# Kernel optimization log

Measured on AMD Instinct MI355X. Metric: run time of the kernel, lower is better.

The kernel has to match this reference:

```python
import jax, jax.numpy as jnp
import numpy as np

SCALE = 0.08838834764831845  # 1/sqrt(head_dim=128)

T, H, D = 8192, 16, 128
NUM_SLOTS = 16384
SEQ_LEN = 2048


def setup_inputs() -> dict:
    key = jax.random.key(0)
    kq, kk, kv = jax.random.split(key, 3)
    q = jax.random.normal(kq, (T, H, D), dtype=jnp.float32)
    k = jax.random.normal(kk, (T, H, D), dtype=jnp.float32)
    v = jax.random.normal(kv, (T, H, D), dtype=jnp.float32)
    k_cache = jnp.zeros((NUM_SLOTS, H * D), dtype=jnp.float32)
    v_cache = jnp.zeros((NUM_SLOTS, H * D), dtype=jnp.float32)
    slot_mapping = jnp.arange(T, dtype=jnp.int32)  # contiguous slots; -1 would mean skip
    return {"q": q, "k": k, "v": v, "k_cache": k_cache, "v_cache": v_cache,
            "slot_mapping": slot_mapping, "seq_len": SEQ_LEN}


def reference(q, k, v, k_cache, v_cache, slot_mapping, seq_len):
    # --- store_kvcache: scatter per-token K/V rows into paged cache slots ---
    t, h, d = q.shape
    num_slots = k_cache.shape[0]
    # slot == -1 means "do not store"; remap to an out-of-bounds index and drop.
    safe_slots = jnp.where(slot_mapping < 0, num_slots, slot_mapping)
    k_cache = k_cache.at[safe_slots].set(k.reshape(t, h * d), mode="drop")
    v_cache = v_cache.at[safe_slots].set(v.reshape(t, h * d), mode="drop")

    # --- prefill attention reading K/V from the cache (block_tables path) ---
    # cu_seqlens = [0, S, 2S, ...]: equal-length sequences packed contiguously,
    # so the per-sequence cache slices are the first t rows reshaped to [B,S,H,D].
    b = t // seq_len
    qb = q.reshape(b, seq_len, h, d)
    kb = k_cache[:t].reshape(b, seq_len, h, d)
    vb = v_cache[:t].reshape(b, seq_len, h, d)

    scores = jnp.einsum("bqhd,bkhd->bhqk", qb, kb) * SCALE  # [B,H,S,S]
    causal = jnp.tril(jnp.ones((seq_len, seq_len), dtype=bool))
    scores = jnp.where(causal[None, None], scores, -jnp.inf)
    p = jax.nn.softmax(scores, axis=-1)
    o = jnp.einsum("bhqk,bkhd->bqhd", p, vb)
    return o.reshape(t, h, d)
```

## Files before the change

kernel.cpp:

```cpp
#include <hip/hip_runtime.h>

typedef float f32x16 __attribute__((ext_vector_type(16)));
typedef __bf16 bf16x8 __attribute__((ext_vector_type(8)));
typedef unsigned int uint2v __attribute__((ext_vector_type(2)));

#define Hh 16
#define Dd 128
#define SEQ 2048
#define HD 2048
#define ATT_C 0.12751743f
#define NEGINF (-__builtin_inff())

__device__ __forceinline__ ushort f2bf(float f) {
    uint u = __builtin_bit_cast(uint, f);
    return (ushort)((u + 0x7FFFu + ((u >> 16) & 1u)) >> 16);
}

__device__ __forceinline__ uint4 pack8(float4 a, float4 b) {
    uint4 u;
    u.x = (uint)f2bf(a.x) | ((uint)f2bf(a.y) << 16);
    u.y = (uint)f2bf(a.z) | ((uint)f2bf(a.w) << 16);
    u.z = (uint)f2bf(b.x) | ((uint)f2bf(b.y) << 16);
    u.w = (uint)f2bf(b.z) | ((uint)f2bf(b.w) << 16);
    return u;
}

__device__ __forceinline__ uint pkbf(float a, float b) {
    return (uint)f2bf(a) | ((uint)f2bf(b) << 16);
}

__device__ __forceinline__ f32x16 zero16() {
    f32x16 v;
#pragma unroll
    for (int i = 0; i < 16; ++i) v[i] = 0.f;
    return v;
}

__device__ __forceinline__ void gll16(const void* g, void* l) {
    __builtin_amdgcn_global_load_lds(
        (const __attribute__((address_space(1))) unsigned int*)g,
        (__attribute__((address_space(3))) unsigned int*)l, 16, 0, 0);
}

__device__ __forceinline__ bf16x8 mkfrag(uint a01, uint a23, uint a45, uint a67, int hi) {
    uint4 u;
#if __has_builtin(__builtin_amdgcn_permlane32_swap)
    uint2v xz = __builtin_amdgcn_permlane32_swap(a01, a45, false, false);
    uint2v yw = __builtin_amdgcn_permlane32_swap(a23, a67, false, false);
    u.x = xz[0]; u.y = yw[0]; u.z = xz[1]; u.w = yw[1];
    (void)hi;
#else
    uint s01 = __shfl_xor(a01, 32), s23 = __shfl_xor(a23, 32);
    uint s45 = __shfl_xor(a45, 32), s67 = __shfl_xor(a67, 32);
    u.x = hi ? s45 : a01;
    u.y = hi ? s67 : a23;
    u.z = hi ? a45 : s01;
    u.w = hi ? a67 : s23;
#endif
    return __builtin_bit_cast(bf16x8, u);
}

__global__ void initinv(int* __restrict__ inv, int T) {
    int i = blockIdx.x * 256 + threadIdx.x;
    if (i < T) inv[i] = -1;
}
__global__ void buildinv(const int* __restrict__ slots, int* __restrict__ inv, int T) {
    int t = blockIdx.x * 256 + threadIdx.x;
    if (t < T) { int s = slots[t]; if (s >= 0 && s < T) inv[s] = t; }
}

__global__ void fusekv(const float* __restrict__ k, const float* __restrict__ v,
                       const float* __restrict__ kc, const float* __restrict__ vc,
                       const int* __restrict__ inv, ushort* __restrict__ ek,
                       ushort* __restrict__ evt) {
    __shared__ int sv[64];
    __shared__ ushort Ks[64][136];
    __shared__ ushort Lt[128][72];
    const int tid = threadIdx.x;
    const int r0 = blockIdx.x * 64, h = blockIdx.y;
    const int b = r0 >> 11, tok0 = r0 & (SEQ - 1);
    const long tb = ((long)(b * Hh + h) * 32 + (tok0 >> 6)) * 8192;
    if (tid < 64) sv[tid] = inv[r0 + tid];
    __syncthreads();
#pragma unroll
    for (int i = 0; i < 4; ++i) {
        int idx = i * 256 + tid, r = idx >> 4, sg = idx & 15;
        int s = sv[r];
        const float* src = (s >= 0 ? k + (long)s * HD : kc + (long)(r0 + r) * HD) + h * Dd + sg * 8;
        float4 A = *(const float4*)src;
        float4 Bv = *(const float4*)(src + 4);
        *(uint4*)&Ks[r][sg * 8] = pack8(A, Bv);
    }
    const int d = tid & 127, hf2 = tid >> 7;
#pragma unroll
    for (int i = 0; i < 8; ++i) {
        const int t = i * 8 + hf2 * 4;
        ushort wv[4];
#pragma unroll
        for (int jj = 0; jj < 4; ++jj) {
            int s = sv[t + jj];
            const float* sp = (s >= 0 ? v + (long)s * HD : vc + (long)(r0 + t + jj) * HD) + h * Dd + d;
            wv[jj] = f2bf(*sp);
        }
        uint2 u;
        u.x = (uint)wv[0] | ((uint)wv[1] << 16);
        u.y = (uint)wv[2] | ((uint)wv[3] << 16);
        *(uint2*)&Lt[d][t] = u;
    }
    __syncthreads();
#pragma unroll
    for (int i = 0; i < 4; ++i) {
        int c = i * 256 + tid, l = c & 31, j = (c >> 5) & 15, hf = c >> 9;
        *(uint4*)(ek + tb + (long)c * 8) = *(const uint4*)&Ks[hf * 32 + l][j * 8];
    }
#pragma unroll
    for (int i = 0; i < 4; ++i) {
        int c = i * 256 + tid, l = c & 31, ch = (c >> 5) & 7, nt = c >> 8;
        *(uint4*)(evt + tb + (long)c * 8) = *(const uint4*)&Lt[nt * 32 + l][ch * 8];
    }
}

__global__ __launch_bounds__(256, 2) void attn32(const float* __restrict__ q,
                                                 const ushort* __restrict__ ek,
                                                 const ushort* __restrict__ evt,
                                                 float* __restrict__ out) {
    __shared__ ushort KV[2][16384];

    const int tid = threadIdx.x;
    const int w = tid >> 6, lane = tid & 63;
    const int l31 = lane & 31, hi = lane >> 5;
    const int g = blockIdx.x;
    const int bh = g & 63, j = g >> 6;
    const int b = bh >> 4, h = bh & 15;
    const int n1 = 2 * (j + 1), ns = 34;
    const long kvbase = (long)bh * 32 * 8192;
    const int koff = hi * 256 + l31 * 8;

    bf16x8 qf[8];
    auto loadq = [&](int qt_) {
        const int qrow = qt_ * 128 + w * 32 + l31;
        const float* qp = q + ((long)(b * SEQ + qrow) * Hh + h) * Dd + hi * 8;
#pragma unroll
        for (int kk = 0; kk < 8; ++kk) {
            float4 A = *(const float4*)(qp + kk * 16);
            float4 Bv = *(const float4*)(qp + kk * 16 + 4);
            A.x *= ATT_C; A.y *= ATT_C; A.z *= ATT_C; A.w *= ATT_C;
            Bv.x *= ATT_C; Bv.y *= ATT_C; Bv.z *= ATT_C; Bv.w *= ATT_C;
            union { uint4 u; bf16x8 v; } cv;
            cv.u = pack8(A, Bv);
            qf[kk] = cv.v;
        }
    };
    auto stage = [&](int nb, int t) {
        const ushort* kg = ek + kvbase + (long)t * 8192 + tid * 8;
        const ushort* vg = evt + kvbase + (long)t * 8192 + tid * 8;
        ushort* kl = &KV[nb][tid * 8];
        ushort* vl = &KV[nb][8192 + tid * 8];
#pragma unroll
        for (int i = 0; i < 4; ++i) {
            gll16(kg + i * 2048, kl + i * 2048);
            gll16(vg + i * 2048, vl + i * 2048);
        }
    };

    f32x16 o[4];
#pragma unroll
    for (int nt = 0; nt < 4; ++nt) o[nt] = zero16();
    float m = NEGINF, lsum = 0.f;

    stage(0, 0);
    loadq(j);
    __syncthreads();

    int cur = 0;
    int qt = j, qtb = qt * 128 + w * 32;

    for (int s = 0; s < ns; ++s) {
        if (s + 1 < ns) stage(cur ^ 1, (s + 1 < n1) ? s + 1 : s + 1 - n1);
        if (s == n1) { qt = 15 - j; qtb = qt * 128 + w * 32; loadq(qt); }
        const int kv0 = ((s < n1) ? s : s - n1) * 64;
        const int qpos = qtb + l31;
        const ushort* Kb = &KV[cur][0];
        const ushort* Vb = &KV[cur][8192];

        if (kv0 <= qtb + 31) {
            const bool h2full = (kv0 + 32 <= qtb + 31);
            f32x16 s0 = zero16(), s1;
            __builtin_amdgcn_s_setprio(1);
#pragma unroll
            for (int kk = 0; kk < 8; ++kk)
                s0 = __builtin_amdgcn_mfma_f32_32x32x16_bf16(
                    *(const bf16x8*)&Kb[kk * 512 + koff], qf[kk], s0, 0, 0, 0);
            if (h2full) {
                s1 = zero16();
#pragma unroll
                for (int kk = 0; kk < 8; ++kk)
                    s1 = __builtin_amdgcn_mfma_f32_32x32x16_bf16(
                        *(const bf16x8*)&Kb[4096 + kk * 512 + koff], qf[kk], s1, 0, 0, 0);
            }
            __builtin_amdgcn_s_setprio(0);

            float mt = NEGINF;
            const bool needmask = (kv0 + 63 > qtb);
            if (needmask) {
#pragma unroll
                for (int r = 0; r < 16; ++r) {
                    const int kr = kv0 + ((r & 3) + 8 * (r >> 2) + 4 * hi);
                    float a0 = (kr <= qpos) ? s0[r] : NEGINF;
                    s0[r] = a0;
                    mt = fmaxf(mt, a0);
                }
                if (h2full) {
#pragma unroll
                    for (int r = 0; r < 16; ++r) {
                        const int kr = kv0 + 32 + ((r & 3) + 8 * (r >> 2) + 4 * hi);
                        float a1 = (kr <= qpos) ? s1[r] : NEGINF;
                        s1[r] = a1;
                        mt = fmaxf(mt, a1);
                    }
                }
            } else {
#pragma unroll
                for (int r = 0; r < 16; ++r) mt = fmaxf(mt, fmaxf(s0[r], s1[r]));
            }
            mt = fmaxf(mt, __shfl_xor(mt, 32));

            if (!__all(mt <= m + 8.f)) {
                const float mn = fmaxf(m, mt);
                const float al = exp2f(m - mn);
                m = mn;
                lsum *= al;
#pragma unroll
                for (int r = 0; r < 16; ++r) {
                    const float alr = __shfl(al, (r & 3) + 8 * (r >> 2) + 4 * hi);
                    o[0][r] *= alr; o[1][r] *= alr; o[2][r] *= alr; o[3][r] *= alr;
                }
            }

            float psum = 0.f;
#pragma unroll
            for (int r = 0; r < 16; ++r) {
                s0[r] = __builtin_amdgcn_exp2f(s0[r] - m);
                psum += s0[r];
            }
            if (h2full) {
#pragma unroll
                for (int r = 0; r < 16; ++r) {
                    s1[r] = __builtin_amdgcn_exp2f(s1[r] - m);
                    psum += s1[r];
                }
            }
            lsum += psum;

            bf16x8 pa00 = mkfrag(pkbf(s0[0], s0[1]), pkbf(s0[2], s0[3]),
                                 pkbf(s0[4], s0[5]), pkbf(s0[6], s0[7]), hi);
            bf16x8 pa01 = mkfrag(pkbf(s0[8], s0[9]), pkbf(s0[10], s0[11]),
                                 pkbf(s0[12], s0[13]), pkbf(s0[14], s0[15]), hi);
            __builtin_amdgcn_s_setprio(1);
#pragma unroll
            for (int nt = 0; nt < 4; ++nt) {
                const int vb = nt * 2048 + koff;
                o[nt] = __builtin_amdgcn_mfma_f32_32x32x16_bf16(
                    pa00, *(const bf16x8*)&Vb[vb], o[nt], 0, 0, 0);
                o[nt] = __builtin_amdgcn_mfma_f32_32x32x16_bf16(
                    pa01, *(const bf16x8*)&Vb[vb + 512], o[nt], 0, 0, 0);
            }
            __builtin_amdgcn_s_setprio(0);
            if (h2full) {
                bf16x8 pa10 = mkfrag(pkbf(s1[0], s1[1]), pkbf(s1[2], s1[3]),
                                     pkbf(s1[4], s1[5]), pkbf(s1[6], s1[7]), hi);
                bf16x8 pa11 = mkfrag(pkbf(s1[8], s1[9]), pkbf(s1[10], s1[11]),
                                     pkbf(s1[12], s1[13]), pkbf(s1[14], s1[15]), hi);
                __builtin_amdgcn_s_setprio(1);
#pragma unroll
                for (int nt = 0; nt < 4; ++nt) {
                    const int vb = nt * 2048 + koff;
                    o[nt] = __builtin_amdgcn_mfma_f32_32x32x16_bf16(
                        pa10, *(const bf16x8*)&Vb[vb + 1024], o[nt], 0, 0, 0);
                    o[nt] = __builtin_amdgcn_mfma_f32_32x32x16_bf16(
                        pa11, *(const bf16x8*)&Vb[vb + 1536], o[nt], 0, 0, 0);
                }
                __builtin_amdgcn_s_setprio(0);
            }
        }

        if (s == n1 - 1 || s == ns - 1) {
            const float lt = lsum + __shfl_xor(lsum, 32);
            const float inv_ = 1.f / lt;
#pragma unroll
            for (int r = 0; r < 16; ++r) {
                const int qr = (r & 3) + 8 * (r >> 2) + 4 * hi;
                const float ivr = __shfl(inv_, qr);
                float* op = out + ((long)(b * SEQ + qtb + qr) * Hh + h) * Dd + l31;
                op[0]  = o[0][r] * ivr;
                op[32] = o[1][r] * ivr;
                op[64] = o[2][r] * ivr;
                op[96] = o[3][r] * ivr;
            }
#pragma unroll
            for (int nt = 0; nt < 4; ++nt) o[nt] = zero16();
            m = NEGINF; lsum = 0.f;
        }

        __syncthreads();
        cur ^= 1;
    }
}

extern "C" void kernel_launch(void* const* d_in, const int* in_sizes, int n_in,
                              void* d_out, int out_size, void* d_ws, size_t ws_size,
                              hipStream_t stream) {
    const float* q = (const float*)d_in[0];
    const float* k = (const float*)d_in[1];
    const float* v = (const float*)d_in[2];
    const float* k_cache = (const float*)d_in[3];
    const float* v_cache = (const float*)d_in[4];
    const int* slot_mapping = (const int*)d_in[5];
    float* out = (float*)d_out;

    const int T = in_sizes[0] / HD;
    (void)n_in; (void)out_size; (void)ws_size;

    ushort* ek = (ushort*)d_ws;
    ushort* evt = ek + (size_t)T * HD;
    int* inv = (int*)(evt + (size_t)T * HD);

    initinv<<<T / 256, 256, 0, stream>>>(inv, T);
    buildinv<<<T / 256, 256, 0, stream>>>(slot_mapping, inv, T);
    fusekv<<<dim3(T / 64, Hh), 256, 0, stream>>>(k, v, k_cache, v_cache, inv, ek, evt);
    attn32<<<dim3(512), 256, 0, stream>>>(q, ek, evt, out);
}
```

Measured before the change: 159.1 us.

## Use 256-row query tiles with 512-thread blocks and hardware bf16 packing

Doubles the query tile per block from 128 to 256 rows by using 8 waves, and halves the grid to 256 blocks. Each staged K/V tile in LDS is therefore shared by twice as many query rows, which cuts global and LDS load traffic per unit of work. The change also replaces the software round-to-nearest bf16 conversion with the v_cvt_pk_bf16_f32 instruction, and interleaves the two QK MFMA chains when both halves are full. The trade-off is fewer blocks to fill the CUs, a coarser causal load-balancing pairing, and more register pressure under the new launch bounds.

```diff
diff --git a/kernel.cpp b/kernel.cpp
--- a/kernel.cpp
+++ b/kernel.cpp
@@ -25,8 +25,10 @@
     return u;
 }
 
-__device__ __forceinline__ uint pkbf(float a, float b) {
-    return (uint)f2bf(a) | ((uint)f2bf(b) << 16);
+__device__ __forceinline__ uint cvtpk(float a, float b) {
+    uint r;
+    asm("v_cvt_pk_bf16_f32 %0, %1, %2" : "=v"(r) : "v"(a), "v"(b));
+    return r;
 }
 
 __device__ __forceinline__ f32x16 zero16() {
@@ -120,7 +122,7 @@
     }
 }
 
-__global__ __launch_bounds__(256, 2) void attn32(const float* __restrict__ q,
+__global__ __launch_bounds__(512, 2) void attn32(const float* __restrict__ q,
                                                  const ushort* __restrict__ ek,
                                                  const ushort* __restrict__ evt,
                                                  float* __restrict__ out) {
@@ -130,15 +132,15 @@
     const int w = tid >> 6, lane = tid & 63;
     const int l31 = lane & 31, hi = lane >> 5;
     const int g = blockIdx.x;
-    const int bh = g & 63, j = g >> 6;
+    const int bh = g & 63, jp = g >> 6;
     const int b = bh >> 4, h = bh & 15;
-    const int n1 = 2 * (j + 1), ns = 34;
+    const int n1 = 4 * (jp + 1), ns = 36;
     const long kvbase = (long)bh * 32 * 8192;
     const int koff = hi * 256 + l31 * 8;
 
     bf16x8 qf[8];
     auto loadq = [&](int qt_) {
-        const int qrow = qt_ * 128 + w * 32 + l31;
+        const int qrow = qt_ * 256 + w * 32 + l31;
         const float* qp = q + ((long)(b * SEQ + qrow) * Hh + h) * Dd + hi * 8;
 #pragma unroll
         for (int kk = 0; kk < 8; ++kk) {
@@ -157,9 +159,9 @@
         ushort* kl = &KV[nb][tid * 8];
         ushort* vl = &KV[nb][8192 + tid * 8];
 #pragma unroll
-        for (int i = 0; i < 4; ++i) {
-            gll16(kg + i * 2048, kl + i * 2048);
-            gll16(vg + i * 2048, vl + i * 2048);
+        for (int i = 0; i < 2; ++i) {
+            gll16(kg + i * 4096, kl + i * 4096);
+            gll16(vg + i * 4096, vl + i * 4096);
         }
     };
 
@@ -169,15 +171,15 @@
     float m = NEGINF, lsum = 0.f;
 
     stage(0, 0);
-    loadq(j);
+    loadq(jp);
     __syncthreads();
 
     int cur = 0;
-    int qt = j, qtb = qt * 128 + w * 32;
+    int qt = jp, qtb = qt * 256 + w * 32;
 
     for (int s = 0; s < ns; ++s) {
         if (s + 1 < ns) stage(cur ^ 1, (s + 1 < n1) ? s + 1 : s + 1 - n1);
-        if (s == n1) { qt = 15 - j; qtb = qt * 128 + w * 32; loadq(qt); }
+        if (s == n1) { qt = 7 - jp; qtb = qt * 256 + w * 32; loadq(qt); }
         const int kv0 = ((s < n1) ? s : s - n1) * 64;
         const int qpos = qtb + l31;
         const ushort* Kb = &KV[cur][0];
@@ -187,16 +189,20 @@
             const bool h2full = (kv0 + 32 <= qtb + 31);
             f32x16 s0 = zero16(), s1;
             __builtin_amdgcn_s_setprio(1);
-#pragma unroll
-            for (int kk = 0; kk < 8; ++kk)
-                s0 = __builtin_amdgcn_mfma_f32_32x32x16_bf16(
-                    *(const bf16x8*)&Kb[kk * 512 + koff], qf[kk], s0, 0, 0, 0);
             if (h2full) {
                 s1 = zero16();
 #pragma unroll
-                for (int kk = 0; kk < 8; ++kk)
+                for (int kk = 0; kk < 8; ++kk) {
+                    s0 = __builtin_amdgcn_mfma_f32_32x32x16_bf16(
+                        *(const bf16x8*)&Kb[kk * 512 + koff], qf[kk], s0, 0, 0, 0);
                     s1 = __builtin_amdgcn_mfma_f32_32x32x16_bf16(
                         *(const bf16x8*)&Kb[4096 + kk * 512 + koff], qf[kk], s1, 0, 0, 0);
+                }
+            } else {
+#pragma unroll
+                for (int kk = 0; kk < 8; ++kk)
+                    s0 = __builtin_amdgcn_mfma_f32_32x32x16_bf16(
+                        *(const bf16x8*)&Kb[kk * 512 + koff], qf[kk], s0, 0, 0, 0);
             }
             __builtin_amdgcn_s_setprio(0);
 
@@ -252,10 +258,10 @@
             }
             lsum += psum;
 
-            bf16x8 pa00 = mkfrag(pkbf(s0[0], s0[1]), pkbf(s0[2], s0[3]),
-                                 pkbf(s0[4], s0[5]), pkbf(s0[6], s0[7]), hi);
-            bf16x8 pa01 = mkfrag(pkbf(s0[8], s0[9]), pkbf(s0[10], s0[11]),
-                                 pkbf(s0[12], s0[13]), pkbf(s0[14], s0[15]), hi);
+            bf16x8 pa00 = mkfrag(cvtpk(s0[0], s0[1]), cvtpk(s0[2], s0[3]),
+                                 cvtpk(s0[4], s0[5]), cvtpk(s0[6], s0[7]), hi);
+            bf16x8 pa01 = mkfrag(cvtpk(s0[8], s0[9]), cvtpk(s0[10], s0[11]),
+                                 cvtpk(s0[12], s0[13]), cvtpk(s0[14], s0[15]), hi);
             __builtin_amdgcn_s_setprio(1);
 #pragma unroll
             for (int nt = 0; nt < 4; ++nt) {
@@ -267,10 +273,10 @@
             }
             __builtin_amdgcn_s_setprio(0);
             if (h2full) {
-                bf16x8 pa10 = mkfrag(pkbf(s1[0], s1[1]), pkbf(s1[2], s1[3]),
-                                     pkbf(s1[4], s1[5]), pkbf(s1[6], s1[7]), hi);
-                bf16x8 pa11 = mkfrag(pkbf(s1[8], s1[9]), pkbf(s1[10], s1[11]),
-                                     pkbf(s1[12], s1[13]), pkbf(s1[14], s1[15]), hi);
+                bf16x8 pa10 = mkfrag(cvtpk(s1[0], s1[1]), cvtpk(s1[2], s1[3]),
+                                     cvtpk(s1[4], s1[5]), cvtpk(s1[6], s1[7]), hi);
+                bf16x8 pa11 = mkfrag(cvtpk(s1[8], s1[9]), cvtpk(s1[10], s1[11]),
+                                     cvtpk(s1[12], s1[13]), cvtpk(s1[14], s1[15]), hi);
                 __builtin_amdgcn_s_setprio(1);
 #pragma unroll
                 for (int nt = 0; nt < 4; ++nt) {
@@ -328,5 +334,5 @@
     initinv<<<T / 256, 256, 0, stream>>>(inv, T);
     buildinv<<<T / 256, 256, 0, stream>>>(slot_mapping, inv, T);
     fusekv<<<dim3(T / 64, Hh), 256, 0, stream>>>(k, v, k_cache, v_cache, inv, ek, evt);
-    attn32<<<dim3(512), 256, 0, stream>>>(q, ek, evt, out);
-}
+    attn32<<<dim3(256), 512, 0, stream>>>(q, ek, evt, out);
+}
```

New measurement: 153.6 us. 3.5% less time.

## Process 64 query rows per wave sharing each K/V fragment across two tiles

Applied to the files above, without the earlier changes.

Each wave now handles two 32-row query tiles (256 query rows per block), so every K and V fragment read from LDS feeds two MFMAs, halving LDS traffic per unit of compute. The paired causal work split (j and 15-j in one block) is replaced by a mapping over 8 row groups per head with a swapped ordering for load balance. The manual bf16 rounding is replaced with the hardware v_cvt_pk_bf16_f32 instruction, and the max/sum reductions use tree order. Doubling the accumulators and Q fragments raises register pressure and may affect occupancy or cause spills, and the new grid likely halves the block count (the launch code is not shown).

```diff
diff --git a/kernel.cpp b/kernel.cpp
--- a/kernel.cpp
+++ b/kernel.cpp
@@ -25,8 +25,10 @@
     return u;
 }
 
-__device__ __forceinline__ uint pkbf(float a, float b) {
-    return (uint)f2bf(a) | ((uint)f2bf(b) << 16);
+__device__ __forceinline__ uint cvtpk(float a, float b) {
+    uint r;
+    asm("v_cvt_pk_bf16_f32 %0, %1, %2" : "=v"(r) : "v"(a), "v"(b));
+    return r;
 }
 
 __device__ __forceinline__ f32x16 zero16() {
@@ -34,6 +36,21 @@
 #pragma unroll
     for (int i = 0; i < 16; ++i) v[i] = 0.f;
     return v;
+}
+
+__device__ __forceinline__ float hmax16(const f32x16 v) {
+    float a0 = fmaxf(v[0], v[1]), a1 = fmaxf(v[2], v[3]);
+    float a2 = fmaxf(v[4], v[5]), a3 = fmaxf(v[6], v[7]);
+    float a4 = fmaxf(v[8], v[9]), a5 = fmaxf(v[10], v[11]);
+    float a6 = fmaxf(v[12], v[13]), a7 = fmaxf(v[14], v[15]);
+    float b0 = fmaxf(a0, a1), b1 = fmaxf(a2, a3), b2 = fmaxf(a4, a5), b3 = fmaxf(a6, a7);
+    return fmaxf(fmaxf(b0, b1), fmaxf(b2, b3));
+}
+__device__ __forceinline__ float hsum16(const f32x16 v) {
+    float a0 = v[0] + v[1], a1 = v[2] + v[3], a2 = v[4] + v[5], a3 = v[6] + v[7];
+    float a4 = v[8] + v[9], a5 = v[10] + v[11], a6 = v[12] + v[13], a7 = v[14] + v[15];
+    float b0 = a0 + a1, b1 = a2 + a3, b2 = a4 + a5, b3 = a6 + a7;
+    return (b0 + b1) + (b2 + b3);
 }
 
 __device__ __forceinline__ void gll16(const void* g, void* l) {
@@ -120,25 +137,90 @@
     }
 }
 
-__global__ __launch_bounds__(256, 2) void attn32(const float* __restrict__ q,
-                                                 const ushort* __restrict__ ek,
-                                                 const ushort* __restrict__ evt,
-                                                 float* __restrict__ out) {
+#define DOHALF(HH)                                                                          \
+  {                                                                                         \
+    const int kadd = (HH) * 4096, vadd = (HH) * 1024;                                       \
+    const int kb0 = kv0 + (HH) * 32;                                                        \
+    f32x16 z0 = zero16(), z1 = zero16();                                                    \
+    __builtin_amdgcn_s_setprio(1);                                                          \
+    _Pragma("unroll")                                                                       \
+    for (int kk = 0; kk < 8; ++kk) {                                                        \
+      bf16x8 kf = *(const bf16x8*)&Kb[kadd + kk * 512 + koff];                              \
+      z0 = __builtin_amdgcn_mfma_f32_32x32x16_bf16(kf, qf0[kk], z0, 0, 0, 0);               \
+      z1 = __builtin_amdgcn_mfma_f32_32x32x16_bf16(kf, qf1[kk], z1, 0, 0, 0);               \
+    }                                                                                       \
+    __builtin_amdgcn_s_setprio(0);                                                          \
+    if (diag) {                                                                             \
+      _Pragma("unroll")                                                                     \
+      for (int r = 0; r < 16; ++r) {                                                        \
+        const int kr = kb0 + ((r & 3) + 8 * (r >> 2) + 4 * hi);                             \
+        z0[r] = (kr <= qp0) ? z0[r] : NEGINF;                                               \
+        z1[r] = (kr <= qp1) ? z1[r] : NEGINF;                                               \
+      }                                                                                     \
+    }                                                                                       \
+    float mt0 = hmax16(z0), mt1 = hmax16(z1);                                               \
+    mt0 = fmaxf(mt0, __shfl_xor(mt0, 32));                                                  \
+    mt1 = fmaxf(mt1, __shfl_xor(mt1, 32));                                                  \
+    if (!(__all(mt0 <= ms0 + 8.f) && __all(mt1 <= ms1 + 8.f))) {                            \
+      const float mn0 = fmaxf(ms0, mt0), mn1 = fmaxf(ms1, mt1);                             \
+      const float al0 = exp2f(ms0 - mn0), al1 = exp2f(ms1 - mn1);                           \
+      ms0 = mn0; ms1 = mn1; ls0 *= al0; ls1 *= al1;                                         \
+      _Pragma("unroll")                                                                     \
+      for (int r = 0; r < 16; ++r) {                                                        \
+        const int pr = (r & 3) + 8 * (r >> 2) + 4 * hi;                                     \
+        const float a0_ = __shfl(al0, pr), a1_ = __shfl(al1, pr);                           \
+        o[0][r] *= a0_; o[1][r] *= a0_; o[2][r] *= a0_; o[3][r] *= a0_;                     \
+        o[4][r] *= a1_; o[5][r] *= a1_; o[6][r] *= a1_; o[7][r] *= a1_;                     \
+      }                                                                                     \
+    }                                                                                       \
+    _Pragma("unroll")                                                                       \
+    for (int r = 0; r < 16; ++r) {                                                          \
+      z0[r] = __builtin_amdgcn_exp2f(z0[r] - ms0);                                          \
+      z1[r] = __builtin_amdgcn_exp2f(z1[r] - ms1);                                          \
+    }                                                                                       \
+    ls0 += hsum16(z0); ls1 += hsum16(z1);                                                   \
+    bf16x8 pa00 = mkfrag(cvtpk(z0[0], z0[1]), cvtpk(z0[2], z0[3]),                          \
+                         cvtpk(z0[4], z0[5]), cvtpk(z0[6], z0[7]), hi);                     \
+    bf16x8 pa01 = mkfrag(cvtpk(z0[8], z0[9]), cvtpk(z0[10], z0[11]),                        \
+                         cvtpk(z0[12], z0[13]), cvtpk(z0[14], z0[15]), hi);                 \
+    bf16x8 pa10 = mkfrag(cvtpk(z1[0], z1[1]), cvtpk(z1[2], z1[3]),                          \
+                         cvtpk(z1[4], z1[5]), cvtpk(z1[6], z1[7]), hi);                     \
+    bf16x8 pa11 = mkfrag(cvtpk(z1[8], z1[9]), cvtpk(z1[10], z1[11]),                        \
+                         cvtpk(z1[12], z1[13]), cvtpk(z1[14], z1[15]), hi);                 \
+    __builtin_amdgcn_s_setprio(1);                                                          \
+    _Pragma("unroll")                                                                       \
+    for (int nt = 0; nt < 4; ++nt) {                                                        \
+      const int vb = nt * 2048 + koff + vadd;                                               \
+      bf16x8 vf0 = *(const bf16x8*)&Vb[vb];                                                 \
+      bf16x8 vf1 = *(const bf16x8*)&Vb[vb + 512];                                           \
+      o[nt]     = __builtin_amdgcn_mfma_f32_32x32x16_bf16(pa00, vf0, o[nt], 0, 0, 0);       \
+      o[nt]     = __builtin_amdgcn_mfma_f32_32x32x16_bf16(pa01, vf1, o[nt], 0, 0, 0);       \
+      o[4 + nt] = __builtin_amdgcn_mfma_f32_32x32x16_bf16(pa10, vf0, o[4 + nt], 0, 0, 0);   \
+      o[4 + nt] = __builtin_amdgcn_mfma_f32_32x32x16_bf16(pa11, vf1, o[4 + nt], 0, 0, 0);   \
+    }                                                                                       \
+    __builtin_amdgcn_s_setprio(0);                                                          \
+  }
+
+__global__ __launch_bounds__(256) __attribute__((amdgpu_waves_per_eu(2)))
+void attn32(const float* __restrict__ q, const ushort* __restrict__ ek,
+            const ushort* __restrict__ evt, float* __restrict__ out) {
     __shared__ ushort KV[2][16384];
 
     const int tid = threadIdx.x;
     const int w = tid >> 6, lane = tid & 63;
     const int l31 = lane & 31, hi = lane >> 5;
     const int g = blockIdx.x;
-    const int bh = g & 63, j = g >> 6;
+    const int bh = g & 63, ig = g >> 6;
+    const int jj = (ig < 4) ? ig : 11 - ig;
     const int b = bh >> 4, h = bh & 15;
-    const int n1 = 2 * (j + 1), ns = 34;
+    const int ns = 4 * (jj + 1);
     const long kvbase = (long)bh * 32 * 8192;
     const int koff = hi * 256 + l31 * 8;
-
-    bf16x8 qf[8];
-    auto loadq = [&](int qt_) {
-        const int qrow = qt_ * 128 + w * 32 + l31;
+    const int qtb = jj * 256 + w * 64;
+    const int qp0 = qtb + l31, qp1 = qtb + 32 + l31;
+
+    bf16x8 qf0[8], qf1[8];
+    auto loadq = [&](int qrow, bf16x8* qf) {
         const float* qp = q + ((long)(b * SEQ + qrow) * Hh + h) * Dd + hi * 8;
 #pragma unroll
         for (int kk = 0; kk < 8; ++kk) {
@@ -163,147 +245,50 @@
         }
     };
 
-    f32x16 o[4];
-#pragma unroll
-    for (int nt = 0; nt < 4; ++nt) o[nt] = zero16();
-    float m = NEGINF, lsum = 0.f;
+    loadq(qtb + l31, qf0);
+    loadq(qtb + 32 + l31, qf1);
+
+    f32x16 o[8];
+#pragma unroll
+    for (int nt = 0; nt < 8; ++nt) o[nt] = zero16();
+    float ms0 = NEGINF, ms1 = NEGINF, ls0 = 0.f, ls1 = 0.f;
 
     stage(0, 0);
-    loadq(j);
     __syncthreads();
 
     int cur = 0;
-    int qt = j, qtb = qt * 128 + w * 32;
-
     for (int s = 0; s < ns; ++s) {
-        if (s + 1 < ns) stage(cur ^ 1, (s + 1 < n1) ? s + 1 : s + 1 - n1);
-        if (s == n1) { qt = 15 - j; qtb = qt * 128 + w * 32; loadq(qt); }
-        const int kv0 = ((s < n1) ? s : s - n1) * 64;
-        const int qpos = qtb + l31;
-        const ushort* Kb = &KV[cur][0];
-        const ushort* Vb = &KV[cur][8192];
-
-        if (kv0 <= qtb + 31) {
-            const bool h2full = (kv0 + 32 <= qtb + 31);
-            f32x16 s0 = zero16(), s1;
-            __builtin_amdgcn_s_setprio(1);
-#pragma unroll
-            for (int kk = 0; kk < 8; ++kk)
-                s0 = __builtin_amdgcn_mfma_f32_32x32x16_bf16(
-                    *(const bf16x8*)&Kb[kk * 512 + koff], qf[kk], s0, 0, 0, 0);
-            if (h2full) {
-                s1 = zero16();
-#pragma unroll
-                for (int kk = 0; kk < 8; ++kk)
-                    s1 = __builtin_amdgcn_mfma_f32_32x32x16_bf16(
-                        *(const bf16x8*)&Kb[4096 + kk * 512 + koff], qf[kk], s1, 0, 0, 0);
-            }
-            __builtin_amdgcn_s_setprio(0);
-
-            float mt = NEGINF;
-            const bool needmask = (kv0 + 63 > qtb);
-            if (needmask) {
-#pragma unroll
-                for (int r = 0; r < 16; ++r) {
-                    const int kr = kv0 + ((r & 3) + 8 * (r >> 2) + 4 * hi);
-                    float a0 = (kr <= qpos) ? s0[r] : NEGINF;
-                    s0[r] = a0;
-                    mt = fmaxf(mt, a0);
-                }
-                if (h2full) {
-#pragma unroll
-                    for (int r = 0; r < 16; ++r) {
-                        const int kr = kv0 + 32 + ((r & 3) + 8 * (r >> 2) + 4 * hi);
-                        float a1 = (kr <= qpos) ? s1[r] : NEGINF;
-                        s1[r] = a1;
-                        mt = fmaxf(mt, a1);
-                    }
-                }
-            } else {
-#pragma unroll
-                for (int r = 0; r < 16; ++r) mt = fmaxf(mt, fmaxf(s0[r], s1[r]));
-            }
-            mt = fmaxf(mt, __shfl_xor(mt, 32));
-
-            if (!__all(mt <= m + 8.f)) {
-                const float mn = fmaxf(m, mt);
-                const float al = exp2f(m - mn);
-                m = mn;
-                lsum *= al;
-#pragma unroll
-                for (int r = 0; r < 16; ++r) {
-                    const float alr = __shfl(al, (r & 3) + 8 * (r >> 2) + 4 * hi);
-                    o[0][r] *= alr; o[1][r] *= alr; o[2][r] *= alr; o[3][r] *= alr;
-                }
-            }
-
-            float psum = 0.f;
-#pragma unroll
-            for (int r = 0; r < 16; ++r) {
-                s0[r] = __builtin_amdgcn_exp2f(s0[r] - m);
-                psum += s0[r];
-            }
-            if (h2full) {
-#pragma unroll
-                for (int r = 0; r < 16; ++r) {
-                    s1[r] = __builtin_amdgcn_exp2f(s1[r] - m);
-                    psum += s1[r];
-                }
-            }
-            lsum += psum;
-
-            bf16x8 pa00 = mkfrag(pkbf(s0[0], s0[1]), pkbf(s0[2], s0[3]),
-                                 pkbf(s0[4], s0[5]), pkbf(s0[6], s0[7]), hi);
-            bf16x8 pa01 = mkfrag(pkbf(s0[8], s0[9]), pkbf(s0[10], s0[11]),
-                                 pkbf(s0[12], s0[13]), pkbf(s0[14], s0[15]), hi);
-            __builtin_amdgcn_s_setprio(1);
-#pragma unroll
-            for (int nt = 0; nt < 4; ++nt) {
-                const int vb = nt * 2048 + koff;
-                o[nt] = __builtin_amdgcn_mfma_f32_32x32x16_bf16(
-                    pa00, *(const bf16x8*)&Vb[vb], o[nt], 0, 0, 0);
-                o[nt] = __builtin_amdgcn_mfma_f32_32x32x16_bf16(
-                    pa01, *(const bf16x8*)&Vb[vb + 512], o[nt], 0, 0, 0);
-            }
-            __builtin_amdgcn_s_setprio(0);
-            if (h2full) {
-                bf16x8 pa10 = mkfrag(pkbf(s1[0], s1[1]), pkbf(s1[2], s1[3]),
-                                     pkbf(s1[4], s1[5]), pkbf(s1[6], s1[7]), hi);
-                bf16x8 pa11 = mkfrag(pkbf(s1[8], s1[9]), pkbf(s1[10], s1[11]),
-                                     pkbf(s1[12], s1[13]), pkbf(s1[14], s1[15]), hi);
-                __builtin_amdgcn_s_setprio(1);
-#pragma unroll
-                for (int nt = 0; nt < 4; ++nt) {
-                    const int vb = nt * 2048 + koff;
-                    o[nt] = __builtin_amdgcn_mfma_f32_32x32x16_bf16(
-                        pa10, *(const bf16x8*)&Vb[vb + 1024], o[nt], 0, 0, 0);
-                    o[nt] = __builtin_amdgcn_mfma_f32_32x32x16_bf16(
-                        pa11, *(const bf16x8*)&Vb[vb + 1536], o[nt], 0, 0, 0);
-                }
-                __builtin_amdgcn_s_setprio(0);
-            }
+        if (s + 1 < ns) stage(cur ^ 1, s + 1);
+        const int kv0 = s * 64;
+        if (kv0 <= qtb + 63) {
+            const ushort* Kb = &KV[cur][0];
+            const ushort* Vb = &KV[cur][8192];
+            const bool diag = (kv0 + 63 > qtb);
+            const bool h2 = (kv0 + 32 <= qtb + 63);
+            DOHALF(0);
+            if (h2) DOHALF(1);
         }
-
-        if (s == n1 - 1 || s == ns - 1) {
-            const float lt = lsum + __shfl_xor(lsum, 32);
-            const float inv_ = 1.f / lt;
-#pragma unroll
-            for (int r = 0; r < 16; ++r) {
-                const int qr = (r & 3) + 8 * (r >> 2) + 4 * hi;
-                const float ivr = __shfl(inv_, qr);
-                float* op = out + ((long)(b * SEQ + qtb + qr) * Hh + h) * Dd + l31;
-                op[0]  = o[0][r] * ivr;
-                op[32] = o[1][r] * ivr;
-                op[64] = o[2][r] * ivr;
-                op[96] = o[3][r] * ivr;
-            }
-#pragma unroll
-            for (int nt = 0; nt < 4; ++nt) o[nt] = zero16();
-            m = NEGINF; lsum = 0.f;
-        }
-
         __syncthreads();
         cur ^= 1;
+    }
+
+    const float lt0 = ls0 + __shfl_xor(ls0, 32);
+    const float lt1 = ls1 + __shfl_xor(ls1, 32);
+    const float iv0 = 1.f / lt0, iv1 = 1.f / lt1;
+#pragma unroll
+    for (int r = 0; r < 16; ++r) {
+        const int qr = (r & 3) + 8 * (r >> 2) + 4 * hi;
+        const float a0 = __shfl(iv0, qr), a1 = __shfl(iv1, qr);
+        float* op0 = out + ((long)(b * SEQ + qtb + qr) * Hh + h) * Dd + l31;
+        float* op1 = out + ((long)(b * SEQ + qtb + 32 + qr) * Hh + h) * Dd + l31;
+        op0[0]  = o[0][r] * a0;
+        op0[32] = o[1][r] * a0;
+        op0[64] = o[2][r] * a0;
+        op0[96] = o[3][r] * a0;
+        op1[0]  = o[4][r] * a1;
+        op1[32] = o[5][r] * a1;
+        op1[64] = o[6][r] * a1;
+        op1[96] = o[7][r] * a1;
     }
 }
 
```

After: 175.2 us. 10.1% more time.
